# Kernel tuning notes

Hardware: AMD Instinct MI355X
Metric: run time of the kernel (lower is better)

The kernel has to match this reference:

```python
import jax, jax.numpy as jnp
import numpy as np

EPS = 1e-8

def _cos_loss(a, b):
    # faithful to torch cos_loss: norm = sqrt(sum(x*x)), x / (norm + 1e-8)
    a_norm = jnp.sqrt(jnp.sum(a * a, axis=1, keepdims=True))
    b_norm = jnp.sqrt(jnp.sum(b * b, axis=1, keepdims=True))
    a_n = a / (a_norm + EPS)
    b_n = b / (b_norm + EPS)
    cossim = jnp.sum(a_n * b_n, axis=1)
    return jnp.mean(1.0 - cossim)

def setup_inputs() -> dict:
    key = jax.random.key(0)
    k1, k2, k3 = jax.random.split(key, 3)
    shape = (1, 768, 64, 64)  # [n, c_cat(block2 VGG16 feats), h, w]
    a = jax.random.normal(k1, shape, dtype=jnp.float32)
    b = jax.random.normal(k2, shape, dtype=jnp.float32)
    d = jax.random.normal(k3, shape, dtype=jnp.float32)
    return {"a": a, "b": b, "d": d}

def reference(a, b, d):
    n, c, h, w = a.shape
    hw = h * w
    a_flat = a.reshape(n, c, hw)   # [n, c, hw]
    b_flat = b.reshape(n, c, hw)   # [n, c, h2w2]
    d_flat = d.reshape(n, c, hw)
    # normalize exactly as argmin_cos_distance: sqrt(sum + 1e-8) then /(norm + 1e-8)
    b_norm = jnp.sqrt(jnp.sum(b_flat * b_flat, axis=1, keepdims=True) + EPS)
    b_n = b_flat / (b_norm + EPS)
    a_norm = jnp.sqrt(jnp.sum(a_flat * a_flat, axis=1, keepdims=True) + EPS)
    a_n = a_flat / (a_norm + EPS)
    # cosine distance matrix [n, hw, h2w2]
    d_mat = 1.0 - jnp.einsum('ncp,ncq->npq', a_n, b_n)
    z_best = jnp.argmin(d_mat, axis=2)  # [n, hw]
    # gather matched style features from d
    idx = jnp.broadcast_to(z_best[:, None, :], (n, c, hw))
    target_feats = jnp.take_along_axis(d_flat, idx, axis=2)  # [n, c, hw]
    # NNFM loss between rendered feats and matched style feats (score is detached)
    loss = _cos_loss(a_flat, target_feats)
    z_new = target_feats.reshape(n, c, h, w)
    return (loss, z_new, z_best)
```

## Files before the change

### kernel.cpp

```cpp
#include <hip/hip_runtime.h>
#include <math.h>

#define EPS  1e-8f
#define C    768
#define HW   4096
#define NKB  24
#define NNB  12
#define NBN  32
#define TAU  0.016f
#define NCH_NEW 12
#define NCH_OLD 48
#define NTT  (3 * (HW / 64) * (C / 64))

typedef float  floatx4 __attribute__((ext_vector_type(4)));
typedef short  shortx8 __attribute__((ext_vector_type(8)));
typedef unsigned short ushort_t;
typedef unsigned int   uint_t;
typedef __attribute__((address_space(1))) uint_t as1_uint;
typedef __attribute__((address_space(3))) uint_t as3_uint;

__device__ __forceinline__ ushort_t f2bf(float v) {
    uint_t u = __float_as_uint(v);
    uint_t r = (u + 0x7FFFu + ((u >> 16) & 1u)) >> 16;
    return (ushort_t)r;
}
__device__ __forceinline__ void async_cp16(const ushort_t* g, ushort_t* l) {
    __builtin_amdgcn_global_load_lds((const as1_uint*)g, (as3_uint*)l, 16, 0, 0);
}

__global__ __launch_bounds__(256) void prep_kernel(
    const float* __restrict__ a, const float* __restrict__ b,
    ushort_t* __restrict__ Ah, ushort_t* __restrict__ Bh,
    float* __restrict__ nbp2, float* __restrict__ out)
{
    __shared__ float tile[64][65];
    const int t = threadIdx.x;
    const int p0 = blockIdx.x * 64;
    const int c0 = blockIdx.y * 64;
    const int r16 = t >> 4;
    const int q4  = (t & 15) * 4;
    const int pl = t >> 2, g = t & 3;
    const int pg = p0 + pl;
    const int sw = (pg >> 1) & 3;

    if (blockIdx.x == 0 && blockIdx.y == 0 && t == 0) out[0] = 0.f;

#pragma unroll
    for (int pp = 0; pp < 4; ++pp) {
        int c = pp * 16 + r16;
        float4 v = *(const float4*)&b[(size_t)(c0 + c) * HW + p0 + q4];
        tile[c][q4]     = v.x; tile[c][q4 + 1] = v.y;
        tile[c][q4 + 2] = v.z; tile[c][q4 + 3] = v.w;
    }
    __syncthreads();
#pragma unroll
    for (int h = 0; h < 2; ++h) {
        const int kb = (c0 >> 5) + h;
        uint_t w[4];
#pragma unroll
        for (int u = 0; u < 4; ++u) {
            ushort_t lo = f2bf(tile[h * 32 + g * 8 + 2 * u][pl]);
            ushort_t hi = f2bf(tile[h * 32 + g * 8 + 2 * u + 1][pl]);
            w[u] = (uint_t)lo | ((uint_t)hi << 16);
        }
        uint4* oh = (uint4*)(Bh + ((size_t)kb * HW + pg) * 32);
        oh[g ^ sw] = make_uint4(w[0], w[1], w[2], w[3]);
    }
    if (t < 64) {
        float s = 0.f;
#pragma unroll
        for (int c = 0; c < 64; ++c) { float v = tile[c][t]; s += v * v; }
        nbp2[blockIdx.y * HW + p0 + t] = s;
    }
    __syncthreads();

#pragma unroll
    for (int pp = 0; pp < 4; ++pp) {
        int c = pp * 16 + r16;
        float4 v = *(const float4*)&a[(size_t)(c0 + c) * HW + p0 + q4];
        tile[c][q4]     = v.x; tile[c][q4 + 1] = v.y;
        tile[c][q4 + 2] = v.z; tile[c][q4 + 3] = v.w;
    }
    __syncthreads();
#pragma unroll
    for (int h = 0; h < 2; ++h) {
        const int kb = (c0 >> 5) + h;
        uint_t w[4];
#pragma unroll
        for (int u = 0; u < 4; ++u) {
            ushort_t lo = f2bf(tile[h * 32 + g * 8 + 2 * u][pl]);
            ushort_t hi = f2bf(tile[h * 32 + g * 8 + 2 * u + 1][pl]);
            w[u] = (uint_t)lo | ((uint_t)hi << 16);
        }
        uint4* oh = (uint4*)(Ah + ((size_t)kb * HW + pg) * 32);
        oh[g ^ sw] = make_uint4(w[0], w[1], w[2], w[3]);
    }
}

__global__ __launch_bounds__(256, 4) void gemm_mfma_kernel(
    const ushort_t* __restrict__ Ah, const ushort_t* __restrict__ Bh,
    const float* __restrict__ nbp2,
    const float* __restrict__ a, const float* __restrict__ b,
    const float* __restrict__ d,
    float* __restrict__ dT, float* __restrict__ bT,
    float* __restrict__ aT, int at_ok,
    float* __restrict__ pv1, int* __restrict__ pi1,
    float* __restrict__ pv2, int* __restrict__ pi2)
{
    __shared__ __align__(16) char smem[33280];
    ushort_t* sA0 = (ushort_t*)smem;
    ushort_t* sB0 = (ushort_t*)(smem + 8192);
    ushort_t* sA1 = (ushort_t*)(smem + 16384);
    ushort_t* sB1 = (ushort_t*)(smem + 24576);
    float*    nb_s = (float*)(smem + 32768);

    const int tid  = threadIdx.x;
    const int lane = tid & 63;
    const int wave = tid >> 6;
    const int wm = wave >> 1, wn = wave & 1;
    const int flat = blockIdx.y * (HW / 128) + blockIdx.x;
    const int orig = (flat & 7) * 128 + (flat >> 3);
    const int bm = orig >> 5, bn = orig & 31;
    const int l15 = lane & 15, l4 = lane >> 4;
    const int swz = (l15 >> 1) & 3;

    floatx4 acc[4][4];
#pragma unroll
    for (int i = 0; i < 4; ++i)
#pragma unroll
        for (int j = 0; j < 4; ++j) acc[i][j] = (floatx4){0.f, 0.f, 0.f, 0.f};

    auto stage = [&](int kb, ushort_t* dA, ushort_t* dB) {
        const size_t aoff = (size_t)(kb * HW + bm * 128) * 32 + tid * 8;
        const size_t boff = (size_t)(kb * HW + bn * 128) * 32 + tid * 8;
        async_cp16(Ah + aoff,        dA + tid * 8);
        async_cp16(Ah + aoff + 2048, dA + tid * 8 + 2048);
        async_cp16(Bh + boff,        dB + tid * 8);
        async_cp16(Bh + boff + 2048, dB + tid * 8 + 2048);
    };
    auto compute = [&](const ushort_t* pA, const ushort_t* pB) {
        shortx8 af[4], bf_[4];
#pragma unroll
        for (int i = 0; i < 4; ++i)
            af[i] = *(const shortx8*)&pA[((wm * 4 + i) * 16 + l15) * 32 + ((l4 ^ swz) * 8)];
#pragma unroll
        for (int j = 0; j < 4; ++j)
            bf_[j] = *(const shortx8*)&pB[((wn * 4 + j) * 16 + l15) * 32 + ((l4 ^ swz) * 8)];
#pragma unroll
        for (int i = 0; i < 4; ++i)
#pragma unroll
            for (int j = 0; j < 4; ++j)
                acc[i][j] = __builtin_amdgcn_mfma_f32_16x16x32_bf16(af[i], bf_[j], acc[i][j], 0, 0, 0);
    };

    stage(0, sA0, sB0);
    if (tid < 128) {
        float s = 0.f;
        int q = bn * 128 + tid;
#pragma unroll
        for (int ch = 0; ch < NNB; ++ch) s += nbp2[ch * HW + q];
        nb_s[tid] = 1.0f / (sqrtf(s + EPS) + EPS);
    }
    __syncthreads();

    for (int kb = 0; kb < NKB; kb += 2) {
        stage(kb + 1, sA1, sB1);
        compute(sA0, sB0);
        __syncthreads();
        if (kb + 2 < NKB) stage(kb + 2, sA0, sB0);
        compute(sA1, sB1);
        __syncthreads();
    }

    float rnb[4];
#pragma unroll
    for (int j = 0; j < 4; ++j)
        rnb[j] = nb_s[wn * 64 + j * 16 + l15];

    float* lv1 = (float*)smem;
    int*   li1 = (int*)(smem + 1024);
    float* lv2 = (float*)(smem + 2048);
    int*   li2 = (int*)(smem + 3072);

#pragma unroll
    for (int i = 0; i < 4; ++i) {
#pragma unroll
        for (int r = 0; r < 4; ++r) {
            float v1 = -INFINITY, v2 = -INFINITY; int i1 = 0, i2 = 0;
#pragma unroll
            for (int j = 0; j < 4; ++j) {
                float sv = acc[i][j][r] * rnb[j];
                int q = bn * 128 + wn * 64 + j * 16 + l15;
                if (sv > v1) { v2 = v1; i2 = i1; v1 = sv; i1 = q; }
                else if (sv > v2) { v2 = sv; i2 = q; }
            }
#pragma unroll
            for (int m = 1; m < 16; m <<= 1) {
                float ov1 = __shfl_xor(v1, m, 64);
                int   oi1 = __shfl_xor(i1, m, 64);
                float ov2 = __shfl_xor(v2, m, 64);
                int   oi2 = __shfl_xor(i2, m, 64);
                if (ov1 > v1 || (ov1 == v1 && oi1 < i1)) {
                    if (v1 > ov2 || (v1 == ov2 && i1 < oi2)) { v2 = v1; i2 = i1; }
                    else { v2 = ov2; i2 = oi2; }
                    v1 = ov1; i1 = oi1;
                } else if (ov1 > v2 || (ov1 == v2 && oi1 < i2)) {
                    v2 = ov1; i2 = oi1;
                }
            }
            if (l15 == 0) {
                int pl = wm * 64 + i * 16 + l4 * 4 + r;
                lv1[pl * 2 + wn] = v1; li1[pl * 2 + wn] = i1;
                lv2[pl * 2 + wn] = v2; li2[pl * 2 + wn] = i2;
            }
        }
    }
    __syncthreads();
    if (tid < 128) {
        float v1 = lv1[tid * 2],     v2 = lv2[tid * 2];
        int   i1 = li1[tid * 2],     i2 = li2[tid * 2];
        float w1 = lv1[tid * 2 + 1], w2 = lv2[tid * 2 + 1];
        int   j1 = li1[tid * 2 + 1], j2 = li2[tid * 2 + 1];
        if (w1 > v1 || (w1 == v1 && j1 < i1)) {
            if (v1 > w2 || (v1 == w2 && i1 < j2)) { v2 = v1; i2 = i1; }
            else { v2 = w2; i2 = j2; }
            v1 = w1; i1 = j1;
        } else if (w1 > v2 || (w1 == v2 && j1 < i2)) {
            v2 = w1; i2 = j1;
        }
        int p = bm * 128 + tid;
        pv1[p * NBN + bn] = v1; pi1[p * NBN + bn] = i1;
        pv2[p * NBN + bn] = v2; pi2[p * NBN + bn] = i2;
    }

    __syncthreads();
    {
        float (*tile)[65] = (float (*)[65])smem;
        const int r16 = tid >> 4;
        const int q4  = (tid & 15) * 4;
        const int flatb = blockIdx.y * (HW / 128) + blockIdx.x;
        for (int tt = flatb; tt < NTT; tt += 1024) {
            const int which = tt / 768;
            const int idx = tt - which * 768;
            if (which == 2 && !at_ok) break;
            const float* src = (which == 0) ? d : ((which == 1) ? b : a);
            float*       dst = (which == 0) ? dT : ((which == 1) ? bT : aT);
            const int tp0 = (idx & 63) * 64;
            const int tc0 = (idx >> 6) * 64;
#pragma unroll
            for (int pp = 0; pp < 4; ++pp) {
                int c = pp * 16 + r16;
                float4 v = *(const float4*)&src[(size_t)(tc0 + c) * HW + tp0 + q4];
                tile[c][q4]     = v.x; tile[c][q4 + 1] = v.y;
                tile[c][q4 + 2] = v.z; tile[c][q4 + 3] = v.w;
            }
            __syncthreads();
#pragma unroll
            for (int pp = 0; pp < 4; ++pp) {
                int p = pp * 16 + r16;
                float4 v;
                v.x = tile[q4][p];     v.y = tile[q4 + 1][p];
                v.z = tile[q4 + 2][p]; v.w = tile[q4 + 3][p];
                *(float4*)&dst[(size_t)(tp0 + p) * C + tc0 + q4] = v;
            }
            __syncthreads();
        }
    }
}

__global__ __launch_bounds__(256) void reduce_recheck_kernel(
    const float* __restrict__ a, const float* __restrict__ b,
    const float* __restrict__ bT, int bt_ok,
    const float* __restrict__ aT, int at_ok,
    const float* __restrict__ pv1, const int* __restrict__ pi1,
    const float* __restrict__ pv2, const int* __restrict__ pi2,
    int* __restrict__ zb, float* __restrict__ out_zbest)
{
    const int wave = threadIdx.x >> 6, lane = threadIdx.x & 63;
    const int p = blockIdx.x * 4 + wave;
    const int tq = lane & 31;

    float v1, v2, candv; int i1, cand;
    if (lane < 32) {
        v1 = pv1[p * NBN + tq]; i1 = pi1[p * NBN + tq]; v2 = pv2[p * NBN + tq];
        cand = i1; candv = v1;
    } else {
        v1 = -INFINITY; v2 = -INFINITY; i1 = 0x7fffffff;
        cand = pi2[p * NBN + tq];
        candv = pv2[p * NBN + tq];
    }
#pragma unroll
    for (int m = 1; m < 32; m <<= 1) {
        float ov1 = __shfl_xor(v1, m, 64);
        int   oi1 = __shfl_xor(i1, m, 64);
        float ov2 = __shfl_xor(v2, m, 64);
        if (ov1 > v1 || (ov1 == v1 && oi1 < i1)) {
            v2 = fmaxf(v1, ov2); v1 = ov1; i1 = oi1;
        } else {
            v2 = fmaxf(v2, ov1);
        }
    }
    v1 = __shfl(v1, 0, 64); v2 = __shfl(v2, 0, 64); i1 = __shfl(i1, 0, 64);

    if (v1 - v2 >= TAU) {
        if (lane == 0) { zb[p] = i1; out_zbest[p] = (float)i1; }
        return;
    }

    const bool active = candv >= v1 - TAU;

    if (at_ok) {
        unsigned long long mset = __ballot(active);
        const float* ar = aT + (size_t)p * C + lane * 12;
        float4 a0 = *(const float4*)ar;
        float4 a1 = *(const float4*)(ar + 4);
        float4 a2v = *(const float4*)(ar + 8);
        float bests = -INFINITY; int bestq = 0x7fffffff;
        while (mset) {
            const int src = __ffsll(mset) - 1;
            mset &= mset - 1;
            const int qc = __shfl(cand, src, 64);
            const float* br = bT + (size_t)qc * C + lane * 12;
            float4 b0 = *(const float4*)br;
            float4 b1 = *(const float4*)(br + 4);
            float4 b2v = *(const float4*)(br + 8);
            float dot = a0.x * b0.x + a0.y * b0.y + a0.z * b0.z + a0.w * b0.w
                      + a1.x * b1.x + a1.y * b1.y + a1.z * b1.z + a1.w * b1.w
                      + a2v.x * b2v.x + a2v.y * b2v.y + a2v.z * b2v.z + a2v.w * b2v.w;
            float bb  = b0.x * b0.x + b0.y * b0.y + b0.z * b0.z + b0.w * b0.w
                      + b1.x * b1.x + b1.y * b1.y + b1.z * b1.z + b1.w * b1.w
                      + b2v.x * b2v.x + b2v.y * b2v.y + b2v.z * b2v.z + b2v.w * b2v.w;
#pragma unroll
            for (int m = 1; m < 64; m <<= 1) {
                dot += __shfl_xor(dot, m, 64);
                bb  += __shfl_xor(bb, m, 64);
            }
            const float s = dot / (sqrtf(bb + EPS) + EPS);
            if (s > bests || (s == bests && qc < bestq)) { bests = s; bestq = qc; }
        }
        if (lane == 0) { zb[p] = bestq; out_zbest[p] = (float)bestq; }
        return;
    }

    int q = cand;
    float dot = 0.f, b2 = 0.f;
    if (active) {
        if (bt_ok) {
            const float* br = bT + (size_t)q * C;
            const float* ap = a + p;
#pragma unroll 4
            for (int c = 0; c < C; c += 4) {
                float4 bv = *(const float4*)(br + c);
                dot += ap[(size_t)c * HW] * bv.x + ap[(size_t)(c + 1) * HW] * bv.y
                     + ap[(size_t)(c + 2) * HW] * bv.z + ap[(size_t)(c + 3) * HW] * bv.w;
                b2  += bv.x * bv.x + bv.y * bv.y + bv.z * bv.z + bv.w * bv.w;
            }
        } else {
#pragma unroll 8
            for (int c = 0; c < C; ++c) {
                float av = a[c * HW + p];
                float bv = b[c * HW + q];
                dot += av * bv; b2 += bv * bv;
            }
        }
    }
    float s = active ? (dot / (sqrtf(b2 + EPS) + EPS)) : -INFINITY;
#pragma unroll
    for (int m = 1; m < 64; m <<= 1) {
        float os = __shfl_xor(s, m, 64);
        int   oq = __shfl_xor(q, m, 64);
        if (os > s || (os == s && oq < q)) { s = os; q = oq; }
    }
    if (lane == 0) { zb[p] = q; out_zbest[p] = (float)q; }
}

__global__ __launch_bounds__(256) void gather_loss_kernel(
    const float* __restrict__ a, const float* __restrict__ dT,
    const int* __restrict__ zb, float* __restrict__ out,
    float* __restrict__ pdot, float* __restrict__ pa2, float* __restrict__ pt2)
{
    __shared__ float tile[32][65];
    __shared__ int qs[32];
    const int t = threadIdx.x;
    const int p0 = blockIdx.x * 32;
    const int c0 = blockIdx.y * 64;
    if (t < 32) qs[t] = zb[p0 + t];
    __syncthreads();

    {
        const int pl = t >> 3, sub = t & 7;
        const float* src = dT + (size_t)qs[pl] * C + c0 + sub * 8;
        float4 v0 = *(const float4*)(src);
        float4 v1 = *(const float4*)(src + 4);
        float* dst = &tile[pl][sub * 8];
        dst[0] = v0.x; dst[1] = v0.y; dst[2] = v0.z; dst[3] = v0.w;
        dst[4] = v1.x; dst[5] = v1.y; dst[6] = v1.z; dst[7] = v1.w;
    }
    __syncthreads();

    const int p = t & 31, cg = t >> 5;
    float dot = 0.f, a2 = 0.f, t2 = 0.f;
#pragma unroll
    for (int i = 0; i < 8; ++i) {
        int cc = cg * 8 + i;
        float tv = tile[p][cc];
        float av = a[(size_t)(c0 + cc) * HW + p0 + p];
        out[1 + (size_t)(c0 + cc) * HW + p0 + p] = tv;
        dot += av * tv; a2 += av * av; t2 += tv * tv;
    }
    __shared__ float r1[256], r2[256], r3[256];
    r1[t] = dot; r2[t] = a2; r3[t] = t2;
    __syncthreads();
    if (t < 32) {
        float fd = 0.f, fa = 0.f, ft = 0.f;
#pragma unroll
        for (int g = 0; g < 8; ++g) {
            fd += r1[t + g * 32];
            fa += r2[t + g * 32];
            ft += r3[t + g * 32];
        }
        pdot[blockIdx.y * HW + p0 + t] = fd;
        pa2[blockIdx.y * HW + p0 + t]  = fa;
        pt2[blockIdx.y * HW + p0 + t]  = ft;
    }
}

__global__ __launch_bounds__(256) void loss_finalize_kernel(
    const float* __restrict__ pdot, const float* __restrict__ pa2,
    const float* __restrict__ pt2, float* __restrict__ out, int nch)
{
    int p4 = (blockIdx.x * 256 + threadIdx.x) * 4;
    float d0 = 0.f, d1 = 0.f, d2 = 0.f, d3 = 0.f;
    float a0 = 0.f, a1 = 0.f, a2 = 0.f, a3 = 0.f;
    float t0 = 0.f, t1 = 0.f, t2 = 0.f, t3 = 0.f;
    for (int ch = 0; ch < nch; ++ch) {
        float4 dv = *(const float4*)&pdot[(size_t)ch * HW + p4];
        float4 av = *(const float4*)&pa2[(size_t)ch * HW + p4];
        float4 tv = *(const float4*)&pt2[(size_t)ch * HW + p4];
        d0 += dv.x; d1 += dv.y; d2 += dv.z; d3 += dv.w;
        a0 += av.x; a1 += av.y; a2 += av.z; a3 += av.w;
        t0 += tv.x; t1 += tv.y; t2 += tv.z; t3 += tv.w;
    }
    float contrib =
        (1.f - d0 / ((sqrtf(a0) + EPS) * (sqrtf(t0) + EPS))) +
        (1.f - d1 / ((sqrtf(a1) + EPS) * (sqrtf(t1) + EPS))) +
        (1.f - d2 / ((sqrtf(a2) + EPS) * (sqrtf(t2) + EPS))) +
        (1.f - d3 / ((sqrtf(a3) + EPS) * (sqrtf(t3) + EPS)));
    __shared__ float red[256];
    red[threadIdx.x] = contrib;
    __syncthreads();
    for (int s = 128; s > 0; s >>= 1) {
        if (threadIdx.x < s) red[threadIdx.x] += red[threadIdx.x + s];
        __syncthreads();
    }
    if (threadIdx.x == 0) atomicAdd(out, red[0] * (1.0f / HW));
}

__global__ __launch_bounds__(256) void bnorm_partial_fb_kernel(
    const float* __restrict__ b, float* __restrict__ nbp)
{
    int q = blockIdx.x * 256 + threadIdx.x;
    int c0 = blockIdx.y * 32;
    float s = 0.f;
#pragma unroll 8
    for (int c = c0; c < c0 + 32; ++c) { float v = b[c * HW + q]; s += v * v; }
    nbp[blockIdx.y * HW + q] = s;
}

__global__ __launch_bounds__(256) void bnorm_finalize_fb_kernel(
    const float* __restrict__ nbp, float* __restrict__ nb)
{
    int q = blockIdx.x * 256 + threadIdx.x;
    float s = 0.f;
#pragma unroll
    for (int ch = 0; ch < NKB; ++ch) s += nbp[ch * HW + q];
    nb[q] = sqrtf(s + EPS) + EPS;
}

__global__ __launch_bounds__(256) void gemm_argmax_fb_kernel(
    const float* __restrict__ A, const float* __restrict__ B,
    const float* __restrict__ nb,
    float* __restrict__ pval, int* __restrict__ pidx)
{
    __shared__ __align__(16) char smem[16384];
    float (*As)[128] = (float (*)[128])smem;
    float (*Bs)[128] = (float (*)[128])(smem + 4096);
    const int m0 = blockIdx.x * 128, q0 = blockIdx.y * 128;
    const int tid = threadIdx.x;
    const int tx = tid & 15, ty = tid >> 4;
    const int lr = tid >> 5, lc = (tid & 31) * 4;
    float acc[8][8] = {};
    for (int k0 = 0; k0 < C; k0 += 8) {
        *(float4*)&As[lr][lc] = *(const float4*)&A[(k0 + lr) * HW + m0 + lc];
        *(float4*)&Bs[lr][lc] = *(const float4*)&B[(k0 + lr) * HW + q0 + lc];
        __syncthreads();
#pragma unroll
        for (int kk = 0; kk < 8; ++kk) {
            float a8[8], b8[8];
            *(float4*)&a8[0] = *(float4*)&As[kk][ty * 8];
            *(float4*)&a8[4] = *(float4*)&As[kk][ty * 8 + 4];
            *(float4*)&b8[0] = *(float4*)&Bs[kk][tx * 8];
            *(float4*)&b8[4] = *(float4*)&Bs[kk][tx * 8 + 4];
#pragma unroll
            for (int i = 0; i < 8; ++i)
#pragma unroll
                for (int j = 0; j < 8; ++j) acc[i][j] += a8[i] * b8[j];
        }
        __syncthreads();
    }
    float nbv[8];
#pragma unroll
    for (int j = 0; j < 8; ++j) nbv[j] = nb[q0 + tx * 8 + j];
    float (*rv)[16] = (float (*)[16])smem;
    int   (*ri)[16] = (int   (*)[16])(smem + 8192);
#pragma unroll
    for (int i = 0; i < 8; ++i) {
        float bv = -INFINITY; int bi = 0;
#pragma unroll
        for (int j = 0; j < 8; ++j) {
            float s = acc[i][j] / nbv[j];
            int q = q0 + tx * 8 + j;
            if (s > bv) { bv = s; bi = q; }
        }
        rv[ty * 8 + i][tx] = bv;
        ri[ty * 8 + i][tx] = bi;
    }
    __syncthreads();
    if (tid < 128) {
        float bv = rv[tid][0]; int bi = ri[tid][0];
#pragma unroll
        for (int t = 1; t < 16; ++t) {
            float v = rv[tid][t]; int ii = ri[tid][t];
            if (v > bv || (v == bv && ii < bi)) { bv = v; bi = ii; }
        }
        pval[(m0 + tid) * NBN + blockIdx.y] = bv;
        pidx[(m0 + tid) * NBN + blockIdx.y] = bi;
    }
}

__global__ __launch_bounds__(256) void reduce_fb_kernel(
    const float* __restrict__ pval, const int* __restrict__ pidx,
    int* __restrict__ zb, float* __restrict__ out_zbest)
{
    int p = blockIdx.x * 256 + threadIdx.x;
    float bv = pval[p * NBN]; int bi = pidx[p * NBN];
#pragma unroll 8
    for (int t = 1; t < NBN; ++t) {
        float v = pval[p * NBN + t]; int ii = pidx[p * NBN + t];
        if (v > bv || (v == bv && ii < bi)) { bv = v; bi = ii; }
    }
    zb[p] = bi;
    out_zbest[p] = (float)bi;
}

__global__ __launch_bounds__(256) void gather_partial_kernel(
    const float* __restrict__ a, const float* __restrict__ d,
    const int* __restrict__ zb, float* __restrict__ out,
    float* __restrict__ pdot, float* __restrict__ pa2, float* __restrict__ pt2)
{
    int p = blockIdx.x * 256 + threadIdx.x;
    int ch = blockIdx.y;
    int c0 = ch * (C / NCH_OLD);
    int q = zb[p];
    float dot = 0.f, a2 = 0.f, t2 = 0.f;
#pragma unroll
    for (int c = c0; c < c0 + C / NCH_OLD; ++c) {
        float av = a[c * HW + p];
        float tv = d[c * HW + q];
        dot += av * tv; a2 += av * av; t2 += tv * tv;
        out[1 + c * HW + p] = tv;
    }
    pdot[ch * HW + p] = dot;
    pa2[ch * HW + p] = a2;
    pt2[ch * HW + p] = t2;
}

extern "C" void kernel_launch(void* const* d_in, const int* in_sizes, int n_in,
                              void* d_out, int out_size, void* d_ws, size_t ws_size,
                              hipStream_t stream) {
    const float* a = (const float*)d_in[0];
    const float* b = (const float*)d_in[1];
    const float* d = (const float*)d_in[2];
    float* out = (float*)d_out;
    float* out_zbest = out + 1 + (size_t)C * HW;

    char* ws = (char*)d_ws;
    size_t off = 0;
    auto alloc = [&](size_t bytes) { void* p = ws + off; off = (off + bytes + 255) & ~(size_t)255; return p; };

    const size_t PACK = (size_t)C * HW * 2;
    ushort_t* Ah = (ushort_t*)alloc(PACK);
    ushort_t* Bh = (ushort_t*)alloc(PACK);
    float* nbp = (float*)alloc((size_t)NKB * HW * 4);
    float* pv1 = (float*)alloc((size_t)HW * NBN * 4);
    int*   pi1 = (int*)alloc((size_t)HW * NBN * 4);
    float* pv2 = (float*)alloc((size_t)HW * NBN * 4);
    int*   pi2 = (int*)alloc((size_t)HW * NBN * 4);
    int*   zb  = (int*)alloc(HW * 4);
    float* pdot = (float*)alloc((size_t)NCH_NEW * HW * 4);
    float* pa2  = (float*)alloc((size_t)NCH_NEW * HW * 4);
    float* pt2  = (float*)alloc((size_t)NCH_NEW * HW * 4);
    float* dT  = (float*)alloc((size_t)C * HW * 4);
    float* bT  = (float*)alloc((size_t)C * HW * 4);
    bool fast = off <= ws_size;
    float* aT  = (float*)alloc((size_t)C * HW * 4);
    int at_ok = (off <= ws_size) ? 1 : 0;

    if (fast) {
        prep_kernel<<<dim3(HW / 64, C / 64), 256, 0, stream>>>(
            a, b, Ah, Bh, nbp, out);
        gemm_mfma_kernel<<<dim3(HW / 128, HW / 128), 256, 0, stream>>>(
            Ah, Bh, nbp, a, b, d, dT, bT, aT, at_ok, pv1, pi1, pv2, pi2);
        reduce_recheck_kernel<<<HW / 4, 256, 0, stream>>>(
            a, b, bT, 1, aT, at_ok, pv1, pi1, pv2, pi2, zb, out_zbest);
        gather_loss_kernel<<<dim3(HW / 32, NCH_NEW), 256, 0, stream>>>(
            a, dT, zb, out, pdot, pa2, pt2);
        loss_finalize_kernel<<<HW / 1024, 256, 0, stream>>>(pdot, pa2, pt2, out, NCH_NEW);
    } else {
        off = 0;
        float* nb = (float*)alloc(HW * 4);
        nbp = (float*)alloc((size_t)NKB * HW * 4);
        pv1 = (float*)alloc((size_t)HW * NBN * 4);
        pi1 = (int*)alloc((size_t)HW * NBN * 4);
        zb  = (int*)alloc(HW * 4);
        float* pdot2 = (float*)alloc((size_t)NCH_OLD * HW * 4);
        float* pa22  = (float*)alloc((size_t)NCH_OLD * HW * 4);
        float* pt22  = (float*)alloc((size_t)NCH_OLD * HW * 4);
        hipMemsetAsync(d_out, 0, sizeof(float), stream);
        bnorm_partial_fb_kernel<<<dim3(HW / 256, NKB), 256, 0, stream>>>(b, nbp);
        bnorm_finalize_fb_kernel<<<HW / 256, 256, 0, stream>>>(nbp, nb);
        gemm_argmax_fb_kernel<<<dim3(HW / 128, HW / 128), 256, 0, stream>>>(a, b, nb, pv1, pi1);
        reduce_fb_kernel<<<HW / 256, 256, 0, stream>>>(pv1, pi1, zb, out_zbest);
        gather_partial_kernel<<<dim3(HW / 256, NCH_OLD), 256, 0, stream>>>(
            a, d, zb, out, pdot2, pa22, pt22);
        loss_finalize_kernel<<<HW / 1024, 256, 0, stream>>>(pdot2, pa22, pt22, out, NCH_OLD);
    }
}
```

Before: 148.8 us.

## Enlarge GEMM tile to 256x256 with 512 threads and triple-buffered async pipeline

Grows the cosine-similarity GEMM block tile from 128x128 to 256x256 and uses 8 waves per block, each computing a 128x64 sub-tile, so every loaded operand is reused more times. Replaces double buffering with a three-stage async-copy ring that uses explicit vmcnt waits and raw barriers, and raises MFMA issue priority during compute. The top-2 partial reduction is remapped so each 256-wide tile still writes two 128-column partial slots. The cost is about 97KB of LDS and more accumulator registers per block, which limits occupancy to about one or two blocks per CU, and only 256 blocks are launched.

```diff
diff --git a/kernel.cpp b/kernel.cpp
--- a/kernel.cpp
+++ b/kernel.cpp
@@ -97,7 +97,7 @@
     }
 }
 
-__global__ __launch_bounds__(256, 4) void gemm_mfma_kernel(
+__global__ __launch_bounds__(512, 2) void gemm_mfma_kernel(
     const ushort_t* __restrict__ Ah, const ushort_t* __restrict__ Bh,
     const float* __restrict__ nbp2,
     const float* __restrict__ a, const float* __restrict__ b,
@@ -107,70 +107,87 @@
     float* __restrict__ pv1, int* __restrict__ pi1,
     float* __restrict__ pv2, int* __restrict__ pi2)
 {
-    __shared__ __align__(16) char smem[33280];
-    ushort_t* sA0 = (ushort_t*)smem;
-    ushort_t* sB0 = (ushort_t*)(smem + 8192);
-    ushort_t* sA1 = (ushort_t*)(smem + 16384);
-    ushort_t* sB1 = (ushort_t*)(smem + 24576);
-    float*    nb_s = (float*)(smem + 32768);
+    __shared__ __align__(16) char smem[99584];
+    ushort_t* sB0 = (ushort_t*)smem;
+    ushort_t* sB1 = (ushort_t*)(smem + 32768);
+    ushort_t* sB2 = (ushort_t*)(smem + 65536);
+    float*    nb_s = (float*)(smem + 98304);
 
     const int tid  = threadIdx.x;
     const int lane = tid & 63;
     const int wave = tid >> 6;
-    const int wm = wave >> 1, wn = wave & 1;
-    const int flat = blockIdx.y * (HW / 128) + blockIdx.x;
-    const int orig = (flat & 7) * 128 + (flat >> 3);
-    const int bm = orig >> 5, bn = orig & 31;
+    const int wm = wave >> 2, wn = wave & 3;
+    const int flat = blockIdx.y * (HW / 256) + blockIdx.x;
+    const int orig = (flat & 7) * 32 + (flat >> 3);
+    const int bm = orig >> 4, bn = orig & 15;
     const int l15 = lane & 15, l4 = lane >> 4;
     const int swz = (l15 >> 1) & 3;
 
-    floatx4 acc[4][4];
-#pragma unroll
-    for (int i = 0; i < 4; ++i)
+    floatx4 acc[8][4];
+#pragma unroll
+    for (int i = 0; i < 8; ++i)
 #pragma unroll
         for (int j = 0; j < 4; ++j) acc[i][j] = (floatx4){0.f, 0.f, 0.f, 0.f};
 
-    auto stage = [&](int kb, ushort_t* dA, ushort_t* dB) {
-        const size_t aoff = (size_t)(kb * HW + bm * 128) * 32 + tid * 8;
-        const size_t boff = (size_t)(kb * HW + bn * 128) * 32 + tid * 8;
-        async_cp16(Ah + aoff,        dA + tid * 8);
-        async_cp16(Ah + aoff + 2048, dA + tid * 8 + 2048);
-        async_cp16(Bh + boff,        dB + tid * 8);
-        async_cp16(Bh + boff + 2048, dB + tid * 8 + 2048);
+    auto stage = [&](int kb, ushort_t* buf) {
+        const size_t aoff = (size_t)(kb * HW + bm * 256) * 32 + tid * 8;
+        const size_t boff = (size_t)(kb * HW + bn * 256) * 32 + tid * 8;
+        async_cp16(Ah + aoff,        buf + tid * 8);
+        async_cp16(Ah + aoff + 4096, buf + tid * 8 + 4096);
+        async_cp16(Bh + boff,        buf + 8192 + tid * 8);
+        async_cp16(Bh + boff + 4096, buf + 8192 + tid * 8 + 4096);
     };
-    auto compute = [&](const ushort_t* pA, const ushort_t* pB) {
-        shortx8 af[4], bf_[4];
-#pragma unroll
-        for (int i = 0; i < 4; ++i)
-            af[i] = *(const shortx8*)&pA[((wm * 4 + i) * 16 + l15) * 32 + ((l4 ^ swz) * 8)];
+    auto compute = [&](const ushort_t* buf) {
+        const ushort_t* pA = buf;
+        const ushort_t* pB = buf + 8192;
+        shortx8 af[8], bf_[4];
+#pragma unroll
+        for (int i = 0; i < 8; ++i)
+            af[i] = *(const shortx8*)&pA[((wm * 8 + i) * 16 + l15) * 32 + ((l4 ^ swz) * 8)];
 #pragma unroll
         for (int j = 0; j < 4; ++j)
             bf_[j] = *(const shortx8*)&pB[((wn * 4 + j) * 16 + l15) * 32 + ((l4 ^ swz) * 8)];
-#pragma unroll
-        for (int i = 0; i < 4; ++i)
+        __builtin_amdgcn_s_setprio(1);
+#pragma unroll
+        for (int i = 0; i < 8; ++i)
 #pragma unroll
             for (int j = 0; j < 4; ++j)
                 acc[i][j] = __builtin_amdgcn_mfma_f32_16x16x32_bf16(af[i], bf_[j], acc[i][j], 0, 0, 0);
+        __builtin_amdgcn_s_setprio(0);
     };
 
-    stage(0, sA0, sB0);
-    if (tid < 128) {
+    stage(0, sB0);
+    stage(1, sB1);
+    if (tid < 256) {
         float s = 0.f;
-        int q = bn * 128 + tid;
+        int q = bn * 256 + tid;
 #pragma unroll
         for (int ch = 0; ch < NNB; ++ch) s += nbp2[ch * HW + q];
         nb_s[tid] = 1.0f / (sqrtf(s + EPS) + EPS);
     }
-    __syncthreads();
-
-    for (int kb = 0; kb < NKB; kb += 2) {
-        stage(kb + 1, sA1, sB1);
-        compute(sA0, sB0);
-        __syncthreads();
-        if (kb + 2 < NKB) stage(kb + 2, sA0, sB0);
-        compute(sA1, sB1);
-        __syncthreads();
-    }
+
+#define KSTEP(KB, CUR, NXT)                                   \
+    asm volatile("s_waitcnt vmcnt(4)" ::: "memory");          \
+    __builtin_amdgcn_s_barrier();                             \
+    __builtin_amdgcn_sched_barrier(0);                        \
+    stage((KB) + 2, NXT);                                     \
+    compute(CUR);
+
+    for (int k3 = 0; k3 < 21; k3 += 3) {
+        KSTEP(k3 + 0, sB0, sB2);
+        KSTEP(k3 + 1, sB1, sB0);
+        KSTEP(k3 + 2, sB2, sB1);
+    }
+    KSTEP(21, sB0, sB2);
+#undef KSTEP
+    asm volatile("s_waitcnt vmcnt(4)" ::: "memory");
+    __builtin_amdgcn_s_barrier();
+    __builtin_amdgcn_sched_barrier(0);
+    compute(sB1);
+    asm volatile("s_waitcnt vmcnt(0)" ::: "memory");
+    __builtin_amdgcn_s_barrier();
+    __builtin_amdgcn_sched_barrier(0);
+    compute(sB2);
 
     float rnb[4];
 #pragma unroll
@@ -178,19 +195,20 @@
         rnb[j] = nb_s[wn * 64 + j * 16 + l15];
 
     float* lv1 = (float*)smem;
-    int*   li1 = (int*)(smem + 1024);
-    float* lv2 = (float*)(smem + 2048);
-    int*   li2 = (int*)(smem + 3072);
-
-#pragma unroll
-    for (int i = 0; i < 4; ++i) {
+    int*   li1 = (int*)(smem + 4096);
+    float* lv2 = (float*)(smem + 8192);
+    int*   li2 = (int*)(smem + 12288);
+    __syncthreads();
+
+#pragma unroll
+    for (int i = 0; i < 8; ++i) {
 #pragma unroll
         for (int r = 0; r < 4; ++r) {
             float v1 = -INFINITY, v2 = -INFINITY; int i1 = 0, i2 = 0;
 #pragma unroll
             for (int j = 0; j < 4; ++j) {
                 float sv = acc[i][j][r] * rnb[j];
-                int q = bn * 128 + wn * 64 + j * 16 + l15;
+                int q = bn * 256 + wn * 64 + j * 16 + l15;
                 if (sv > v1) { v2 = v1; i2 = i1; v1 = sv; i1 = q; }
                 else if (sv > v2) { v2 = sv; i2 = q; }
             }
@@ -209,18 +227,20 @@
                 }
             }
             if (l15 == 0) {
-                int pl = wm * 64 + i * 16 + l4 * 4 + r;
-                lv1[pl * 2 + wn] = v1; li1[pl * 2 + wn] = i1;
-                lv2[pl * 2 + wn] = v2; li2[pl * 2 + wn] = i2;
-            }
-        }
-    }
-    __syncthreads();
-    if (tid < 128) {
-        float v1 = lv1[tid * 2],     v2 = lv2[tid * 2];
-        int   i1 = li1[tid * 2],     i2 = li2[tid * 2];
-        float w1 = lv1[tid * 2 + 1], w2 = lv2[tid * 2 + 1];
-        int   j1 = li1[tid * 2 + 1], j2 = li2[tid * 2 + 1];
+                int row = wm * 128 + i * 16 + l4 * 4 + r;
+                lv1[row * 4 + wn] = v1; li1[row * 4 + wn] = i1;
+                lv2[row * 4 + wn] = v2; li2[row * 4 + wn] = i2;
+            }
+        }
+    }
+    __syncthreads();
+    {
+        const int row = tid >> 1, pair = tid & 1;
+        const int base = row * 4 + pair * 2;
+        float v1 = lv1[base],     v2 = lv2[base];
+        int   i1 = li1[base],     i2 = li2[base];
+        float w1 = lv1[base + 1], w2 = lv2[base + 1];
+        int   j1 = li1[base + 1], j2 = li2[base + 1];
         if (w1 > v1 || (w1 == v1 && j1 < i1)) {
             if (v1 > w2 || (v1 == w2 && i1 < j2)) { v2 = v1; i2 = i1; }
             else { v2 = w2; i2 = j2; }
@@ -228,9 +248,10 @@
         } else if (w1 > v2 || (w1 == v2 && j1 < i2)) {
             v2 = w1; i2 = j1;
         }
-        int p = bm * 128 + tid;
-        pv1[p * NBN + bn] = v1; pi1[p * NBN + bn] = i1;
-        pv2[p * NBN + bn] = v2; pi2[p * NBN + bn] = i2;
+        const int p = bm * 256 + row;
+        const int tile = bn * 2 + pair;
+        pv1[p * NBN + tile] = v1; pi1[p * NBN + tile] = i1;
+        pv2[p * NBN + tile] = v2; pi2[p * NBN + tile] = i2;
     }
 
     __syncthreads();
@@ -238,8 +259,8 @@
         float (*tile)[65] = (float (*)[65])smem;
         const int r16 = tid >> 4;
         const int q4  = (tid & 15) * 4;
-        const int flatb = blockIdx.y * (HW / 128) + blockIdx.x;
-        for (int tt = flatb; tt < NTT; tt += 1024) {
+        const int flatb = blockIdx.y * (HW / 256) + blockIdx.x;
+        for (int tt = flatb; tt < NTT; tt += 256) {
             const int which = tt / 768;
             const int idx = tt - which * 768;
             if (which == 2 && !at_ok) break;
@@ -248,16 +269,16 @@
             const int tp0 = (idx & 63) * 64;
             const int tc0 = (idx >> 6) * 64;
 #pragma unroll
-            for (int pp = 0; pp < 4; ++pp) {
-                int c = pp * 16 + r16;
+            for (int pp = 0; pp < 2; ++pp) {
+                int c = pp * 32 + r16;
                 float4 v = *(const float4*)&src[(size_t)(tc0 + c) * HW + tp0 + q4];
                 tile[c][q4]     = v.x; tile[c][q4 + 1] = v.y;
                 tile[c][q4 + 2] = v.z; tile[c][q4 + 3] = v.w;
             }
             __syncthreads();
 #pragma unroll
-            for (int pp = 0; pp < 4; ++pp) {
-                int p = pp * 16 + r16;
+            for (int pp = 0; pp < 2; ++pp) {
+                int p = pp * 32 + r16;
                 float4 v;
                 v.x = tile[q4][p];     v.y = tile[q4 + 1][p];
                 v.z = tile[q4 + 2][p]; v.w = tile[q4 + 3][p];
@@ -609,7 +630,7 @@
     if (fast) {
         prep_kernel<<<dim3(HW / 64, C / 64), 256, 0, stream>>>(
             a, b, Ah, Bh, nbp, out);
-        gemm_mfma_kernel<<<dim3(HW / 128, HW / 128), 256, 0, stream>>>(
+        gemm_mfma_kernel<<<dim3(HW / 256, HW / 256), 512, 0, stream>>>(
             Ah, Bh, nbp, a, b, d, dT, bT, aT, at_ok, pv1, pi1, pv2, pi2);
         reduce_recheck_kernel<<<HW / 4, 256, 0, stream>>>(
             a, b, bT, 1, aT, at_ok, pv1, pi1, pv2, pi2, zb, out_zbest);
```

Result: slower. 166.1 us (+11.6%).
